# Optimization experiments

Hardware: AMD Instinct MI355X
Metric: run time of the kernel (lower is better)

The kernel has to match this reference:

```python
import jax, jax.numpy as jnp
import numpy as np
from jax import lax

B, T, E, D = 32, 4096, 512, 512     # batch, x_steps, eunits, dunits
A, C, F = 128, 32, 15               # attn_dim, conv_channel, aconv_filts
K = 2 * F + 1                       # location conv kernel size
NEG = -1e9


def setup_inputs() -> dict:
    key = jax.random.key(0)
    ks = jax.random.split(key, 12)
    value = jax.random.normal(ks[0], (B, T, E), dtype=jnp.float32)
    value_length = jax.random.randint(ks[1], (B,), T // 2, T + 1).astype(jnp.int32)
    query = jax.random.normal(ks[2], (B, D), dtype=jnp.float32)
    # dirac initialization per initialize_weights()
    prev_attn_weight = jax.nn.one_hot(jnp.zeros((B,), jnp.int32), T, dtype=jnp.float32)
    accum_attn_weight = prev_attn_weight
    s = 0.02
    Wv = jax.random.normal(ks[3], (E, A), dtype=jnp.float32) * s
    bv = jnp.zeros((A,), jnp.float32)
    Wq = jax.random.normal(ks[4], (D, A), dtype=jnp.float32) * s
    conv_k = jax.random.normal(ks[5], (K, 1, C), dtype=jnp.float32) * s  # WIO
    Wl = jax.random.normal(ks[6], (C, A), dtype=jnp.float32) * s
    att_v = jax.random.normal(ks[7], (A,), dtype=jnp.float32)
    att_g = jnp.asarray(np.sqrt(1.0 / A), jnp.float32)
    att_b = jnp.zeros((A,), jnp.float32)
    score_bias = jnp.asarray(0.0, jnp.float32)
    return {"value": value, "value_length": value_length, "query": query,
            "accum_attn_weight": accum_attn_weight, "prev_attn_weight": prev_attn_weight,
            "Wv": Wv, "bv": bv, "Wq": Wq, "conv_k": conv_k, "Wl": Wl,
            "att_v": att_v, "att_g": att_g, "att_b": att_b, "score_bias": score_bias}


def _forward(value, value_length, query, accum_attn_weight, prev_attn_weight,
             Wv, bv, Wq, conv_k, Wl, att_v, att_g, att_b, score_bias):
    # projections
    densed_value = value @ Wv + bv                      # [B,T,A]
    densed_query = (query @ Wq)[:, None, :]             # [B,1,A]
    # location conv over accumulated weights, channels_last SAME
    loc = lax.conv_general_dilated(accum_attn_weight[:, :, None], conv_k,
                                   window_strides=(1,), padding='SAME',
                                   dimension_numbers=('NWC', 'WIO', 'NWC'))  # [B,T,C]
    attn_location = loc @ Wl                            # [B,T,A]
    # weight-normalized energy
    normed_v = att_g * att_v * lax.rsqrt(jnp.sum(jnp.square(att_v)))
    x = attn_location + densed_value + densed_query
    energy = jnp.einsum('bta,a->bt', jnp.tanh(x + att_b), normed_v) + score_bias
    mask = jnp.arange(T)[None, :] < value_length[:, None]
    energy = energy + (1.0 - mask.astype(energy.dtype)) * NEG
    # soft stepwise monotonic update (training=False: no sigmoid noise)
    p = jax.nn.sigmoid(energy)                          # [B,T]
    shifted = jnp.concatenate(
        [jnp.zeros((value.shape[0], 1), p.dtype),
         prev_attn_weight[:, :-1] * (1.0 - p[:, :-1])], axis=1)
    attn_weight = prev_attn_weight * p + shifted        # [B,T]
    attn_c = jnp.einsum('bt,bte->be', attn_weight, value)
    return attn_c, attn_weight


def reference(value, value_length, query, accum_attn_weight, prev_attn_weight,
              Wv, bv, Wq, conv_k, Wl, att_v, att_g, att_b, score_bias):
    return _forward(value, value_length, query, accum_attn_weight, prev_attn_weight,
                    Wv, bv, Wq, conv_k, Wl, att_v, att_g, att_b, score_bias)
```

## Files before the change

### kernel.cpp

```cpp
#include <hip/hip_runtime.h>
#include <hip/hip_bf16.h>

#define TT 4096
#define EE 512
#define AA 128

typedef short short8 __attribute__((ext_vector_type(8)));
typedef float f32x4 __attribute__((ext_vector_type(4)));

__device__ __forceinline__ short f2bf(float f) {
    union { float f; unsigned u; } v; v.f = f;
    unsigned r = v.u + 0x7fffu + ((v.u >> 16) & 1u);
    return (short)(r >> 16);
}

#define WS_WVT   0
#define WS_QBIAS 139264
#define WS_NV    155648
#define WS_P     156160
#define WS_PART  680448

__global__ void prep_kernel(const float* __restrict__ Wv, const float* __restrict__ conv_k,
                            const float* __restrict__ Wl, const float* __restrict__ query,
                            const float* __restrict__ Wq, const float* __restrict__ bv,
                            const float* __restrict__ att_b, const float* __restrict__ att_v,
                            const float* __restrict__ att_g,
                            short* __restrict__ wvt, float* __restrict__ q_bias,
                            float* __restrict__ nv) {
    if (blockIdx.x < 272) {
        int idx = blockIdx.x * 256 + threadIdx.x;
        int a = idx / 544, k = idx % 544;
        float val = 0.f;
        if (k < 512) {
            val = Wv[k * 128 + a];
        } else if (k < 543) {
            int kk = k - 512;
            float s = 0.f;
            #pragma unroll
            for (int c = 0; c < 32; ++c) s += conv_k[kk * 32 + c] * Wl[c * 128 + a];
            val = s;
        }
        wvt[a * 544 + k] = f2bf(val);
    } else {
        int b = blockIdx.x - 272, a = threadIdx.x;
        if (a < 128) {
            float s = 0.f;
            for (int d = 0; d < 512; ++d) s += query[b * 512 + d] * Wq[d * 128 + a];
            q_bias[b * 128 + a] = s + bv[a] + att_b[a];
            if (b == 0) {
                float ss = 0.f;
                #pragma unroll
                for (int i = 0; i < 128; ++i) { float t = att_v[i]; ss += t * t; }
                nv[a] = att_g[0] * att_v[a] * rsqrtf(ss);
            }
        }
    }
}

__global__ __launch_bounds__(256) void energy_kernel(
    const float* __restrict__ value, const int* __restrict__ vlen,
    const float* __restrict__ accum, const short* __restrict__ wvt,
    const float* __restrict__ q_bias, const float* __restrict__ nv,
    const float* __restrict__ score_bias, float* __restrict__ p_buf) {

    int bid = blockIdx.x;
    int b  = bid >> 6;
    int t0 = (bid & 63) << 6;
    int tid = threadIdx.x;
    int w = tid >> 6;
    int l = tid & 63;
    int l15 = l & 15, g = l >> 4;

    int len = vlen[b];
    if (t0 >= len) {
        if (tid < 64) p_buf[b * TT + t0 + tid] = 0.f;
        return;
    }

    int row = t0 + w * 16 + l15;

    f32x4 acc[8];
    #pragma unroll
    for (int i = 0; i < 8; ++i) acc[i] = (f32x4){0.f, 0.f, 0.f, 0.f};

    const float* arow = value + ((size_t)(b * TT + row)) * EE + g * 8;
    const short* brow = wvt + l15 * 544 + g * 8;

    #pragma unroll 4
    for (int kc = 0; kc < 16; ++kc) {
        const float4* ap = (const float4*)(arow + kc * 32);
        float4 v0 = ap[0], v1 = ap[1];
        short8 af;
        af[0] = f2bf(v0.x); af[1] = f2bf(v0.y); af[2] = f2bf(v0.z); af[3] = f2bf(v0.w);
        af[4] = f2bf(v1.x); af[5] = f2bf(v1.y); af[6] = f2bf(v1.z); af[7] = f2bf(v1.w);
        #pragma unroll
        for (int t8 = 0; t8 < 8; ++t8) {
            short8 bf = *(const short8*)(brow + t8 * 16 * 544 + kc * 32);
            acc[t8] = __builtin_amdgcn_mfma_f32_16x16x32_bf16(af, bf, acc[t8], 0, 0, 0);
        }
    }

    {
        short8 af;
        #pragma unroll
        for (int i = 0; i < 8; ++i) {
            int kk = g * 8 + i;
            int t = row - 15 + kk;
            float v = (kk < 31 && t >= 0 && t < TT) ? accum[b * TT + t] : 0.f;
            af[i] = f2bf(v);
        }
        #pragma unroll
        for (int t8 = 0; t8 < 8; ++t8) {
            short8 bf = *(const short8*)(brow + t8 * 16 * 544 + 512);
            acc[t8] = __builtin_amdgcn_mfma_f32_16x16x32_bf16(af, bf, acc[t8], 0, 0, 0);
        }
    }

    float qb[8], nvv[8];
    #pragma unroll
    for (int t8 = 0; t8 < 8; ++t8) {
        int a = t8 * 16 + l15;
        qb[t8]  = q_bias[b * 128 + a];
        nvv[t8] = nv[a];
    }
    float sb = score_bias[0];
    #pragma unroll
    for (int j = 0; j < 4; ++j) {
        float e = 0.f;
        #pragma unroll
        for (int t8 = 0; t8 < 8; ++t8)
            e += tanhf(acc[t8][j] + qb[t8]) * nvv[t8];
        e += __shfl_xor(e, 1);
        e += __shfl_xor(e, 2);
        e += __shfl_xor(e, 4);
        e += __shfl_xor(e, 8);
        if (l15 == 0) {
            int t = t0 + w * 16 + g * 4 + j;
            float p = 0.f;
            if (t < len) { float ee = e + sb; p = 1.f / (1.f + expf(-ee)); }
            p_buf[b * TT + t] = p;
        }
    }
}

__global__ void weight_kernel(const float* __restrict__ p_buf, const float* __restrict__ prev,
                              float* __restrict__ outw) {
    int i = blockIdx.x * 256 + threadIdx.x;
    int t = i & (TT - 1);
    float w = prev[i] * p_buf[i];
    if (t > 0) w += prev[i - 1] * (1.f - p_buf[i - 1]);
    outw[i] = w;
}

__global__ __launch_bounds__(256) void ctx_partial(const float* __restrict__ value,
                                                   const float* __restrict__ wbuf,
                                                   float* __restrict__ part) {
    __shared__ float wsm[512];
    int b = blockIdx.x, tc = blockIdx.y;
    int tid = threadIdx.x;
    wsm[tid]       = wbuf[b * TT + tc * 512 + tid];
    wsm[tid + 256] = wbuf[b * TT + tc * 512 + tid + 256];
    __syncthreads();
    float ax = 0.f, ay = 0.f;
    const float* vbase = value + ((size_t)b * TT + tc * 512) * EE + tid * 2;
    for (int tt = 0; tt < 512; ++tt) {
        float wv = wsm[tt];
        if (wv != 0.f) {
            float2 v = *(const float2*)(vbase + (size_t)tt * EE);
            ax += wv * v.x; ay += wv * v.y;
        }
    }
    float2 r; r.x = ax; r.y = ay;
    *(float2*)(part + ((b * 8 + tc) * 512) + tid * 2) = r;
}

__global__ void ctx_reduce(const float* __restrict__ part, float* __restrict__ outc) {
    int idx = blockIdx.x * 256 + threadIdx.x;
    int b = idx >> 9, e = idx & 511;
    float s = 0.f;
    #pragma unroll
    for (int tc = 0; tc < 8; ++tc) s += part[(b * 8 + tc) * 512 + e];
    outc[idx] = s;
}

extern "C" void kernel_launch(void* const* d_in, const int* in_sizes, int n_in,
                              void* d_out, int out_size, void* d_ws, size_t ws_size,
                              hipStream_t stream) {
    const float* value  = (const float*)d_in[0];
    const int*   vlen   = (const int*)  d_in[1];
    const float* query  = (const float*)d_in[2];
    const float* accum  = (const float*)d_in[3];
    const float* prev   = (const float*)d_in[4];
    const float* Wv     = (const float*)d_in[5];
    const float* bv     = (const float*)d_in[6];
    const float* Wq     = (const float*)d_in[7];
    const float* conv_k = (const float*)d_in[8];
    const float* Wl     = (const float*)d_in[9];
    const float* att_v  = (const float*)d_in[10];
    const float* att_g  = (const float*)d_in[11];
    const float* att_b  = (const float*)d_in[12];
    const float* sbias  = (const float*)d_in[13];

    char* wsb = (char*)d_ws;
    short* wvt   = (short*)(wsb + WS_WVT);
    float* qbias = (float*)(wsb + WS_QBIAS);
    float* nv    = (float*)(wsb + WS_NV);
    float* pbuf  = (float*)(wsb + WS_P);
    float* part  = (float*)(wsb + WS_PART);

    float* outc = (float*)d_out;
    float* outw = (float*)d_out + 32 * 512;

    prep_kernel<<<304, 256, 0, stream>>>(Wv, conv_k, Wl, query, Wq, bv, att_b,
                                         att_v, att_g, wvt, qbias, nv);
    energy_kernel<<<2048, 256, 0, stream>>>(value, vlen, accum, wvt, qbias, nv, sbias, pbuf);
    weight_kernel<<<512, 256, 0, stream>>>(pbuf, prev, outw);
    ctx_partial<<<dim3(32, 8), 256, 0, stream>>>(value, outw, part);
    ctx_reduce <<<64, 256, 0, stream>>>(part, outc);
}
```

Baseline: 503.8 us.

## Stage energy GEMM through double-buffered LDS, fuse weight update into context kernel

The energy kernel now processes 128 rows per block. It stages bf16-converted value tiles and Wv tiles in double-buffered shared memory, with register prefetch of the next k-chunk. This replaces per-wave global loads of the B operand and gives better reuse. The weight update kernel is merged into the context partial kernel, which also skips 64-row chunks whose weights are all zero. The query projection in prep is split across two half-block reductions. In exchange the code adds shared memory and barriers and runs fewer energy blocks.

```diff
diff --git a/kernel.cpp b/kernel.cpp
--- a/kernel.cpp
+++ b/kernel.cpp
@@ -12,6 +12,11 @@
     union { float f; unsigned u; } v; v.f = f;
     unsigned r = v.u + 0x7fffu + ((v.u >> 16) & 1u);
     return (short)(r >> 16);
+}
+__device__ __forceinline__ unsigned pk2bf(float lo, float hi) {
+    __hip_bfloat162 h = __float22bfloat162_rn(make_float2(lo, hi));
+    union { __hip_bfloat162 h; unsigned u; } c; c.h = h;
+    return c.u;
 }
 
 #define WS_WVT   0
@@ -42,11 +47,18 @@
         }
         wvt[a * 544 + k] = f2bf(val);
     } else {
-        int b = blockIdx.x - 272, a = threadIdx.x;
-        if (a < 128) {
-            float s = 0.f;
-            for (int d = 0; d < 512; ++d) s += query[b * 512 + d] * Wq[d * 128 + a];
-            q_bias[b * 128 + a] = s + bv[a] + att_b[a];
+        __shared__ float tmp[2][128];
+        int b = blockIdx.x - 272;
+        int a = threadIdx.x & 127, h = threadIdx.x >> 7;
+        const float* q = query + b * 512 + h * 256;
+        const float* wq = Wq + (h * 256) * 128 + a;
+        float s = 0.f;
+        #pragma unroll 4
+        for (int d = 0; d < 256; ++d) s += q[d] * wq[d * 128];
+        tmp[h][a] = s;
+        __syncthreads();
+        if (threadIdx.x < 128) {
+            q_bias[b * 128 + a] = tmp[0][a] + tmp[1][a] + bv[a] + att_b[a];
             if (b == 0) {
                 float ss = 0.f;
                 #pragma unroll
@@ -57,15 +69,18 @@
     }
 }
 
-__global__ __launch_bounds__(256) void energy_kernel(
+__global__ __launch_bounds__(256, 3) void energy_kernel(
     const float* __restrict__ value, const int* __restrict__ vlen,
     const float* __restrict__ accum, const short* __restrict__ wvt,
     const float* __restrict__ q_bias, const float* __restrict__ nv,
     const float* __restrict__ score_bias, float* __restrict__ p_buf) {
 
+    __shared__ __align__(16) short As[2][128 * 40];
+    __shared__ __align__(16) short Bs[2][128 * 40];
+
     int bid = blockIdx.x;
-    int b  = bid >> 6;
-    int t0 = (bid & 63) << 6;
+    int b  = bid >> 5;
+    int t0 = (bid & 31) << 7;
     int tid = threadIdx.x;
     int w = tid >> 6;
     int l = tid & 63;
@@ -73,34 +88,70 @@
 
     int len = vlen[b];
     if (t0 >= len) {
-        if (tid < 64) p_buf[b * TT + t0 + tid] = 0.f;
+        if (tid < 128) p_buf[b * TT + t0 + tid] = 0.f;
         return;
     }
 
-    int row = t0 + w * 16 + l15;
-
-    f32x4 acc[8];
-    #pragma unroll
-    for (int i = 0; i < 8; ++i) acc[i] = (f32x4){0.f, 0.f, 0.f, 0.f};
-
-    const float* arow = value + ((size_t)(b * TT + row)) * EE + g * 8;
-    const short* brow = wvt + l15 * 544 + g * 8;
-
-    #pragma unroll 4
+    int arow[4], agrn[4];
+    const float* abase[4];
+    #pragma unroll
+    for (int i = 0; i < 4; ++i) {
+        int fl = tid + 256 * i;
+        arow[i] = fl >> 3; agrn[i] = fl & 7;
+        abase[i] = value + ((size_t)(b * TT + t0 + arow[i])) * EE + agrn[i] * 4;
+    }
+    int ba = tid >> 1, bh = (tid & 1) * 16;
+    const short* bbase = wvt + ba * 544 + bh;
+
+    f32x4 acc[2][8];
+    #pragma unroll
+    for (int rt = 0; rt < 2; ++rt)
+        #pragma unroll
+        for (int i = 0; i < 8; ++i) acc[rt][i] = (f32x4){0.f, 0.f, 0.f, 0.f};
+
+    float4 av[4];
+    short8 bv0, bv1;
+    #pragma unroll
+    for (int i = 0; i < 4; ++i) av[i] = *(const float4*)(abase[i]);
+    bv0 = *(const short8*)(bbase);
+    bv1 = *(const short8*)(bbase + 8);
+
+    int cur = 0;
     for (int kc = 0; kc < 16; ++kc) {
-        const float4* ap = (const float4*)(arow + kc * 32);
-        float4 v0 = ap[0], v1 = ap[1];
-        short8 af;
-        af[0] = f2bf(v0.x); af[1] = f2bf(v0.y); af[2] = f2bf(v0.z); af[3] = f2bf(v0.w);
-        af[4] = f2bf(v1.x); af[5] = f2bf(v1.y); af[6] = f2bf(v1.z); af[7] = f2bf(v1.w);
-        #pragma unroll
-        for (int t8 = 0; t8 < 8; ++t8) {
-            short8 bf = *(const short8*)(brow + t8 * 16 * 544 + kc * 32);
-            acc[t8] = __builtin_amdgcn_mfma_f32_16x16x32_bf16(af, bf, acc[t8], 0, 0, 0);
-        }
-    }
-
-    {
+        #pragma unroll
+        for (int i = 0; i < 4; ++i) {
+            uint2 pk;
+            pk.x = pk2bf(av[i].x, av[i].y);
+            pk.y = pk2bf(av[i].z, av[i].w);
+            *(uint2*)(&As[cur][arow[i] * 40 + agrn[i] * 4]) = pk;
+        }
+        *(short8*)(&Bs[cur][ba * 40 + bh])     = bv0;
+        *(short8*)(&Bs[cur][ba * 40 + bh + 8]) = bv1;
+
+        if (kc < 15) {
+            #pragma unroll
+            for (int i = 0; i < 4; ++i) av[i] = *(const float4*)(abase[i] + (kc + 1) * 32);
+            bv0 = *(const short8*)(bbase + (kc + 1) * 32);
+            bv1 = *(const short8*)(bbase + (kc + 1) * 32 + 8);
+        }
+        __syncthreads();
+
+        #pragma unroll
+        for (int rt = 0; rt < 2; ++rt) {
+            short8 af = *(const short8*)(&As[cur][(w * 32 + rt * 16 + l15) * 40 + g * 8]);
+            #pragma unroll
+            for (int t8 = 0; t8 < 8; ++t8) {
+                short8 bf = *(const short8*)(&Bs[cur][(t8 * 16 + l15) * 40 + g * 8]);
+                acc[rt][t8] = __builtin_amdgcn_mfma_f32_16x16x32_bf16(af, bf, acc[rt][t8], 0, 0, 0);
+            }
+        }
+        cur ^= 1;
+        __syncthreads();
+    }
+
+    #pragma unroll
+    for (int rt = 0; rt < 2; ++rt) {
+        int row = t0 + w * 32 + rt * 16 + l15;
         short8 af;
         #pragma unroll
         for (int i = 0; i < 8; ++i) {
@@ -111,8 +162,8 @@
         }
         #pragma unroll
         for (int t8 = 0; t8 < 8; ++t8) {
-            short8 bf = *(const short8*)(brow + t8 * 16 * 544 + 512);
-            acc[t8] = __builtin_amdgcn_mfma_f32_16x16x32_bf16(af, bf, acc[t8], 0, 0, 0);
+            short8 bf = *(const short8*)(wvt + (t8 * 16 + l15) * 544 + 512 + g * 8);
+            acc[rt][t8] = __builtin_amdgcn_mfma_f32_16x16x32_bf16(af, bf, acc[rt][t8], 0, 0, 0);
         }
     }
 
@@ -125,49 +176,65 @@
     }
     float sb = score_bias[0];
     #pragma unroll
-    for (int j = 0; j < 4; ++j) {
-        float e = 0.f;
-        #pragma unroll
-        for (int t8 = 0; t8 < 8; ++t8)
-            e += tanhf(acc[t8][j] + qb[t8]) * nvv[t8];
-        e += __shfl_xor(e, 1);
-        e += __shfl_xor(e, 2);
-        e += __shfl_xor(e, 4);
-        e += __shfl_xor(e, 8);
-        if (l15 == 0) {
-            int t = t0 + w * 16 + g * 4 + j;
-            float p = 0.f;
-            if (t < len) { float ee = e + sb; p = 1.f / (1.f + expf(-ee)); }
-            p_buf[b * TT + t] = p;
-        }
-    }
-}
-
-__global__ void weight_kernel(const float* __restrict__ p_buf, const float* __restrict__ prev,
-                              float* __restrict__ outw) {
-    int i = blockIdx.x * 256 + threadIdx.x;
-    int t = i & (TT - 1);
-    float w = prev[i] * p_buf[i];
-    if (t > 0) w += prev[i - 1] * (1.f - p_buf[i - 1]);
-    outw[i] = w;
-}
-
-__global__ __launch_bounds__(256) void ctx_partial(const float* __restrict__ value,
-                                                   const float* __restrict__ wbuf,
-                                                   float* __restrict__ part) {
+    for (int rt = 0; rt < 2; ++rt) {
+        #pragma unroll
+        for (int j = 0; j < 4; ++j) {
+            float e = 0.f;
+            #pragma unroll
+            for (int t8 = 0; t8 < 8; ++t8)
+                e += tanhf(acc[rt][t8][j] + qb[t8]) * nvv[t8];
+            e += __shfl_xor(e, 1);
+            e += __shfl_xor(e, 2);
+            e += __shfl_xor(e, 4);
+            e += __shfl_xor(e, 8);
+            if (l15 == 0) {
+                int t = t0 + w * 32 + rt * 16 + g * 4 + j;
+                float p = 0.f;
+                if (t < len) { float ee = e + sb; p = 1.f / (1.f + expf(-ee)); }
+                p_buf[b * TT + t] = p;
+            }
+        }
+    }
+}
+
+__global__ __launch_bounds__(256) void ctx_fused(const float* __restrict__ value,
+                                                 const float* __restrict__ p_buf,
+                                                 const float* __restrict__ prev,
+                                                 float* __restrict__ outw,
+                                                 float* __restrict__ part) {
     __shared__ float wsm[512];
+    __shared__ int flags[8];
     int b = blockIdx.x, tc = blockIdx.y;
     int tid = threadIdx.x;
-    wsm[tid]       = wbuf[b * TT + tc * 512 + tid];
-    wsm[tid + 256] = wbuf[b * TT + tc * 512 + tid + 256];
+    if (tid < 8) flags[tid] = 0;
     __syncthreads();
+
+    int tl = tid * 2;
+    {
+        int t = tc * 512 + tl;
+        int gi = b * TT + t;
+        float w0 = prev[gi] * p_buf[gi];
+        if (t > 0) w0 += prev[gi - 1] * (1.f - p_buf[gi - 1]);
+        float w1 = prev[gi + 1] * p_buf[gi + 1] + prev[gi] * (1.f - p_buf[gi]);
+        outw[gi] = w0; outw[gi + 1] = w1;
+        wsm[tl] = w0; wsm[tl + 1] = w1;
+        if (w0 != 0.f) flags[tl >> 6] = 1;
+        if (w1 != 0.f) flags[(tl + 1) >> 6] = 1;
+    }
+    __syncthreads();
+
     float ax = 0.f, ay = 0.f;
     const float* vbase = value + ((size_t)b * TT + tc * 512) * EE + tid * 2;
-    for (int tt = 0; tt < 512; ++tt) {
-        float wv = wsm[tt];
-        if (wv != 0.f) {
-            float2 v = *(const float2*)(vbase + (size_t)tt * EE);
-            ax += wv * v.x; ay += wv * v.y;
+    for (int c = 0; c < 8; ++c) {
+        if (flags[c]) {
+            #pragma unroll 4
+            for (int tt = c * 64; tt < c * 64 + 64; ++tt) {
+                float wv = wsm[tt];
+                if (wv != 0.f) {
+                    float2 v = *(const float2*)(vbase + (size_t)tt * EE);
+                    ax += wv * v.x; ay += wv * v.y;
+                }
+            }
         }
     }
     float2 r; r.x = ax; r.y = ay;
@@ -213,8 +280,7 @@
 
     prep_kernel<<<304, 256, 0, stream>>>(Wv, conv_k, Wl, query, Wq, bv, att_b,
                                          att_v, att_g, wvt, qbias, nv);
-    energy_kernel<<<2048, 256, 0, stream>>>(value, vlen, accum, wvt, qbias, nv, sbias, pbuf);
-    weight_kernel<<<512, 256, 0, stream>>>(pbuf, prev, outw);
-    ctx_partial<<<dim3(32, 8), 256, 0, stream>>>(value, outw, part);
+    energy_kernel<<<1024, 256, 0, stream>>>(value, vlen, accum, wvt, qbias, nv, sbias, pbuf);
+    ctx_fused<<<dim3(32, 8), 256, 0, stream>>>(value, pbuf, prev, outw, part);
     ctx_reduce <<<64, 256, 0, stream>>>(part, outc);
 }
```

New measurement: 424.4 us. 1.19x faster.
